# Kernel optimization log

Hardware: AMD Instinct MI355X
Metric: run time of the kernel (lower is better)

The kernel has to match this reference:

```python
import jax, jax.numpy as jnp
import numpy as np

B, S, D = 32, 512, 1024
H, HD = 16, 64          # num_heads, head_dim
K = 64                  # downsampling_k
NEG = -9e15             # -9000000000000000.0 in source


def setup_inputs() -> dict:
    key0 = jax.random.key(0)
    ks = jax.random.split(key0, 8)
    glorot = lambda k, shape, fan: jax.random.uniform(k, shape, jnp.float32,
                                                      -np.sqrt(6.0 / fan), np.sqrt(6.0 / fan))
    fan = D + H * HD  # glorot_uniform over (hidden, heads*head_dim)
    return {
        "query": jax.random.normal(ks[0], (B, S, D), jnp.float32),
        "key": jax.random.normal(ks[1], (B, S, D), jnp.float32),
        "value": jax.random.normal(ks[2], (B, S, D), jnp.float32),
        "query_kernel": glorot(ks[3], (D, H, HD), fan),
        "key_kernel": glorot(ks[4], (D, H, HD), fan),
        "value_kernel": glorot(ks[5], (D, H, HD), fan),
        "key_downsample_mat": (1.0 / K) * jax.random.normal(ks[6], (K, S), jnp.float32),
        "value_downsample_mat": (1.0 / K) * jax.random.normal(ks[7], (K, S), jnp.float32),
    }


def reference(query, key, value, query_kernel, key_kernel, value_kernel,
              key_downsample_mat, value_downsample_mat):
    # Linformer-style downsampling of K/V along the sequence axis: [B,S,D] -> [B,K,D]
    key_ds = jnp.einsum('ks,bsd->bkd', key_downsample_mat, key)
    val_ds = jnp.einsum('ks,bsd->bkd', value_downsample_mat, value)

    # Per-head projections
    q = jnp.einsum('bsd,dnh->bsnh', query, query_kernel)   # [B,S,H,HD]
    k = jnp.einsum('bkd,dnh->bknh', key_ds, key_kernel)    # [B,K,H,HD]
    v = jnp.einsum('bkd,dnh->bknh', val_ds, value_kernel)  # [B,K,H,HD]

    # Masked softmax attention over the downsampled key set
    scores = jnp.einsum('bqnh,bknh->bnqk', q, k)           # [B,H,S,K]
    # Source builds tril over [S, K_down] then slices first K cols (no-op here)
    mask = jnp.tril(jnp.ones((S, K), dtype=bool))          # [S,K], broadcasts over B,H
    scores = jnp.where(mask, scores, NEG)
    attn = jax.nn.softmax(scores, axis=-1)                 # dropout deterministic (train=False)

    a_v = jnp.einsum('bnqk,bknh->bqnh', attn, v)           # [B,S,H,HD]
    return a_v.reshape(B, S, H * HD)
```

## Files before the change

kernel.cpp:

```cpp
#include <hip/hip_runtime.h>
#include <stdint.h>

#define B_   32
#define S_   512
#define D_   1024
#define H_   16
#define HD_  64
#define KD_  64
#define NH_  1024

typedef __attribute__((ext_vector_type(8))) short short8;
typedef __attribute__((ext_vector_type(4))) float floatx4;

#define GAS __attribute__((address_space(1)))
#define LAS __attribute__((address_space(3)))

__device__ __forceinline__ ushort f2bf(float f) {
  uint32_t u = __float_as_uint(f);
  u = u + 0x7FFFu + ((u >> 16) & 1u);
  return (ushort)(u >> 16);
}

__device__ __forceinline__ float bf2f(ushort h) {
  return __uint_as_float(((uint32_t)h) << 16);
}

__device__ __forceinline__ void gload_lds16(const void* g, void* l) {
  __builtin_amdgcn_global_load_lds((const GAS uint32_t*)g, (LAS uint32_t*)l, 16, 0, 0);
}

#define BARRIER() asm volatile("s_barrier" ::: "memory")
#define WAITLGKM() asm volatile("s_waitcnt lgkmcnt(0)" ::: "memory")

__global__ __launch_bounds__(256) void cvt_split(const float* __restrict__ kdm,
                                                 const float* __restrict__ vdm,
                                                 ushort* __restrict__ hi,
                                                 ushort* __restrict__ lo) {
  int i = blockIdx.x * 256 + threadIdx.x;
  const float* src = (i < 8192) ? kdm : vdm;
  int j = i & 8191;
  float4 v = ((const float4*)src)[j];
  ushort4 h, l;
  h.x = f2bf(v.x); l.x = f2bf(v.x - bf2f(h.x));
  h.y = f2bf(v.y); l.y = f2bf(v.y - bf2f(h.y));
  h.z = f2bf(v.z); l.z = f2bf(v.z - bf2f(h.z));
  h.w = f2bf(v.w); l.w = f2bf(v.w - bf2f(h.w));
  ((ushort4*)hi)[i] = h;
  ((ushort4*)lo)[i] = l;
}

__global__ __launch_bounds__(256, 6) void pre_kv(
    const float* __restrict__ key, const float* __restrict__ value,
    const float* __restrict__ kkm, const float* __restrict__ vkm,
    const ushort* __restrict__ dsm_hi, const ushort* __restrict__ dsm_lo,
    ushort* __restrict__ kkT, ushort* __restrict__ vkT,
    ushort* __restrict__ outk, ushort* __restrict__ outv) {
  __shared__ __align__(16) char smem[26624];
  const int blk = blockIdx.x;
  const int tid = threadIdx.x;

  if (blk < 512) {
    const int bz = (blk & 7) + ((blk >> 6) << 3);
    const int t  = (blk >> 3) & 7;
    const int z = bz >> 5, b = bz & 31;
    const int c0 = t * 128;
    const float* in = z ? value : key;
    ushort* out     = z ? outv : outk;
    const ushort* Ah = dsm_hi + (size_t)z * (KD_ * S_);
    const ushort* Al = dsm_lo + (size_t)z * (KD_ * S_);

    ushort* lAh = (ushort*)smem;
    ushort* lAl = (ushort*)(smem + 4096);
    uint*   lBh = (uint*)(smem + 8192);
    uint*   lBl = (uint*)(smem + 17408);

    const int lane = tid & 63, w = tid >> 6;
    const int lr = lane & 15, lg = lane >> 4;
    const int wn = w * 32;
    const int lam = tid & 31;
    const int d0 = lam * 4;
    const int sp = tid >> 5;

    floatx4 acc[4][2];
#pragma unroll
    for (int m = 0; m < 4; ++m)
#pragma unroll
      for (int n = 0; n < 2; ++n) acc[m][n] = (floatx4){0.f, 0.f, 0.f, 0.f};

    for (int k0 = 0; k0 < S_; k0 += 32) {
      {
        size_t src = (size_t)(tid >> 2) * S_ + k0 + (size_t)(tid & 3) * 8;
        gload_lds16(Ah + src, lAh + w * 512);
        gload_lds16(Al + src, lAl + w * 512);
      }
      float4 ra[2], rb[2];
#pragma unroll
      for (int si = 0; si < 2; ++si) {
        int s = sp * 2 + si * 16;
        const float* p = in + ((size_t)(b * S_ + k0 + s)) * D_ + c0 + d0;
        ra[si] = *(const float4*)p;
        rb[si] = *(const float4*)(p + D_);
      }
      const int swz = lam & 12;
#pragma unroll
      for (int si = 0; si < 2; ++si) {
        int col = (sp + si * 8) ^ swz;
        const float* pa = (const float*)&ra[si];
        const float* pb = (const float*)&rb[si];
#pragma unroll
        for (int i = 0; i < 4; ++i) {
          ushort h0 = f2bf(pa[i]);
          ushort l0 = f2bf(pa[i] - bf2f(h0));
          ushort h1 = f2bf(pb[i]);
          ushort l1 = f2bf(pb[i] - bf2f(h1));
          lBh[(d0 + i) * 18 + col] = (uint)h0 | ((uint)h1 << 16);
          lBl[(d0 + i) * 18 + col] = (uint)l0 | ((uint)l1 << 16);
        }
      }
      __syncthreads();
      short8 bh[2], bl[2];
#pragma unroll
      for (int n = 0; n < 2; ++n) {
        int d = wn + n * 16 + lr;
        int off = d * 18 + ((lg * 4) ^ ((d >> 2) & 12));
        bh[n] = *(const short8*)&lBh[off];
        bl[n] = *(const short8*)&lBl[off];
      }
#pragma unroll
      for (int m = 0; m < 4; ++m) {
        int aoff = (m * 16 + lr) * 32 + lg * 8;
        short8 ah = *(const short8*)&lAh[aoff];
        short8 al = *(const short8*)&lAl[aoff];
#pragma unroll
        for (int n = 0; n < 2; ++n) {
          acc[m][n] = __builtin_amdgcn_mfma_f32_16x16x32_bf16(ah, bh[n], acc[m][n], 0, 0, 0);
          acc[m][n] = __builtin_amdgcn_mfma_f32_16x16x32_bf16(ah, bl[n], acc[m][n], 0, 0, 0);
          acc[m][n] = __builtin_amdgcn_mfma_f32_16x16x32_bf16(al, bh[n], acc[m][n], 0, 0, 0);
        }
      }
      __syncthreads();
    }
    size_t obase = (size_t)b * KD_ * D_;
#pragma unroll
    for (int m = 0; m < 4; ++m)
#pragma unroll
      for (int n = 0; n < 2; ++n)
#pragma unroll
        for (int r = 0; r < 4; ++r)
          out[obase + (size_t)(m * 16 + lg * 4 + r) * D_ + c0 + wn + n * 16 + lr] =
              f2bf(acc[m][n][r]);

  } else {
    const int blk2 = blk - 512;
    const int tz = blk2 >> 10;
    const int rem = blk2 & 1023;
    const int tyb = rem >> 5;
    const int txb = rem & 31;
    const float* in = tz == 0 ? kkm : vkm;
    ushort* outp    = tz == 0 ? kkT : vkT;
    float (*tile)[33] = (float(*)[33])smem;
    const int tx = tid & 31, ty = tid >> 5;
    int x = txb * 32 + tx;
    int y0 = tyb * 32;
#pragma unroll
    for (int j = 0; j < 4; ++j)
      tile[ty + j * 8][tx] = in[(size_t)(y0 + ty + j * 8) * 1024 + x];
    __syncthreads();
    int x2 = tyb * 32 + tx;
    int y2 = txb * 32;
#pragma unroll
    for (int j = 0; j < 4; ++j)
      outp[(size_t)(y2 + ty + j * 8) * 1024 + x2] = f2bf(tile[tx][ty + j * 8]);
  }
}

__global__ __launch_bounds__(256) void gemm_kv_q(
    const ushort* __restrict__ A,
    const ushort* __restrict__ Bt,
    const ushort* __restrict__ Bt2,
    ushort* __restrict__ C,
    const float* __restrict__ qk, ushort* __restrict__ qkT,
    const float* __restrict__ query, ushort* __restrict__ q_bf) {
  __shared__ __align__(16) char smem[16384];
  const int blk = blockIdx.x;
  const int tid = threadIdx.x;

  if (blk < 256) {
    ushort* lA = (ushort*)smem;
    ushort* lB = (ushort*)(smem + 8192);
    int xcd = blk & 7, slot = blk >> 3;
    int mt = xcd * 4 + (slot >> 3);
    int nt = slot & 7;
    int m0 = mt * 128, n0 = nt * 128;
    const ushort* Bsel = (mt >= 16) ? Bt2 : Bt;

    int lane = tid & 63, w = tid >> 6;
    int lr = lane & 15, lg = lane >> 4;
    int wm = (w >> 1) * 64, wn = (w & 1) * 64;
    floatx4 acc[4][4];
#pragma unroll
    for (int m = 0; m < 4; ++m)
#pragma unroll
      for (int n = 0; n < 4; ++n) acc[m][n] = (floatx4){0.f, 0.f, 0.f, 0.f};

    for (int k0 = 0; k0 < 1024; k0 += 32) {
#pragma unroll
      for (int i = 0; i < 2; ++i) {
        int c = i * 256 + w * 64 + lane;
        gload_lds16(A + ((size_t)(m0 + (c >> 2)) * 1024 + k0 + (c & 3) * 8),
                    &lA[(i * 256 + w * 64) * 8]);
        gload_lds16(Bsel + ((size_t)(n0 + (c >> 2)) * 1024 + k0 + (c & 3) * 8),
                    &lB[(i * 256 + w * 64) * 8]);
      }
      __syncthreads();
      short8 af[4], bfr[4];
#pragma unroll
      for (int m = 0; m < 4; ++m)
        af[m] = *(const short8*)&lA[(wm + m * 16 + lr) * 32 + lg * 8];
#pragma unroll
      for (int n = 0; n < 4; ++n)
        bfr[n] = *(const short8*)&lB[(wn + n * 16 + lr) * 32 + lg * 8];
#pragma unroll
      for (int m = 0; m < 4; ++m)
#pragma unroll
        for (int n = 0; n < 4; ++n)
          acc[m][n] = __builtin_amdgcn_mfma_f32_16x16x32_bf16(af[m], bfr[n], acc[m][n], 0, 0, 0);
      __syncthreads();
    }
#pragma unroll
    for (int m = 0; m < 4; ++m)
#pragma unroll
      for (int n = 0; n < 4; ++n)
#pragma unroll
        for (int r = 0; r < 4; ++r)
          C[(size_t)(m0 + wm + m * 16 + lg * 4 + r) * 1024 + n0 + wn + n * 16 + lr] =
              f2bf(acc[m][n][r]);

  } else if (blk < 256 + 1024) {
    const int blk2 = blk - 256;
    const int tyb = blk2 >> 5;
    const int txb = blk2 & 31;
    float (*tile)[33] = (float(*)[33])smem;
    const int tx = tid & 31, ty = tid >> 5;
    int x = txb * 32 + tx;
    int y0 = tyb * 32;
#pragma unroll
    for (int j = 0; j < 4; ++j)
      tile[ty + j * 8][tx] = qk[(size_t)(y0 + ty + j * 8) * 1024 + x];
    __syncthreads();
    int x2 = tyb * 32 + tx;
    int y2 = txb * 32;
#pragma unroll
    for (int j = 0; j < 4; ++j)
      qkT[(size_t)(y2 + ty + j * 8) * 1024 + x2] = f2bf(tile[tx][ty + j * 8]);

  } else {
    const size_t base = (size_t)(blk - 1280) * 2048 + tid;
#pragma unroll
    for (int j = 0; j < 8; ++j) {
      size_t i = base + (size_t)j * 256;
      float4 v = ((const float4*)query)[i];
      ushort4 o;
      o.x = f2bf(v.x); o.y = f2bf(v.y); o.z = f2bf(v.z); o.w = f2bf(v.w);
      ((ushort4*)q_bf)[i] = o;
    }
  }
}

__global__ __launch_bounds__(512, 2) void gemm256_attn(
    const ushort* __restrict__ A, const ushort* __restrict__ Bt,
    const ushort* __restrict__ kp, const ushort* __restrict__ vp,
    float* __restrict__ out) {
  extern __shared__ ushort lds[];
  ushort* ldsA = lds;
  ushort* ldsB = lds + 2 * 256 * 64;
  const int tid = threadIdx.x;
  const int w = tid >> 6, lane = tid & 63;
  const int lr = lane & 15, lg = lane >> 4;
  const int wm = w >> 2, wn = w & 3;
  const int bid = blockIdx.x;
  const int mt = (bid & 7) * 8 + ((bid >> 3) >> 2);
  const int nt = (bid >> 3) & 3;
  const int m0 = mt * 256, n0 = nt * 256;
  const int NT = 16;

  const int srow = tid >> 3;
  const int sslot = tid & 7;

  auto stageA = [&](int sl, int ch, int k0) {
    int rloc = ch * 64 + srow;
    int gs = sslot ^ (rloc & 7);
    gload_lds16(A + (size_t)(m0 + rloc) * 1024 + k0 + gs * 8,
                ldsA + sl * (256 * 64) + ch * (64 * 64) + w * 512);
  };
  auto stageB = [&](int sl, int ch, int k0) {
    int rloc = ch * 64 + srow;
    int gs = sslot ^ (rloc & 7);
    gload_lds16(Bt + (size_t)(n0 + rloc) * 1024 + k0 + gs * 8,
                ldsB + sl * (256 * 64) + ch * (64 * 64) + w * 512);
  };

  short8 af[4][2], bf[2][2];
  auto loadA = [&](int sl, int mh) {
#pragma unroll
    for (int i = 0; i < 4; ++i) {
      int row = wm * 128 + (mh * 4 + i) * 16 + lr;
#pragma unroll
      for (int kk = 0; kk < 2; ++kk) {
        int col = (((kk * 4 + lg) ^ (row & 7)) * 8);
        af[i][kk] = *(const short8*)&ldsA[sl * (256 * 64) + row * 64 + col];
      }
    }
  };
  auto loadB = [&](int sl, int nh) {
#pragma unroll
    for (int j = 0; j < 2; ++j) {
      int row = wn * 64 + (nh * 2 + j) * 16 + lr;
#pragma unroll
      for (int kk = 0; kk < 2; ++kk) {
        int col = (((kk * 4 + lg) ^ (row & 7)) * 8);
        bf[j][kk] = *(const short8*)&ldsB[sl * (256 * 64) + row * 64 + col];
      }
    }
  };

  floatx4 acc[8][4];
#pragma unroll
  for (int i = 0; i < 8; ++i)
#pragma unroll
    for (int j = 0; j < 4; ++j) acc[i][j] = (floatx4){0.f, 0.f, 0.f, 0.f};

  auto mma16 = [&](int mh, int nh) {
    __builtin_amdgcn_s_setprio(1);
#pragma unroll
    for (int i = 0; i < 4; ++i)
#pragma unroll
      for (int j = 0; j < 2; ++j)
#pragma unroll
        for (int kk = 0; kk < 2; ++kk)
          acc[mh * 4 + i][nh * 2 + j] = __builtin_amdgcn_mfma_f32_16x16x32_bf16(
              af[i][kk], bf[j][kk], acc[mh * 4 + i][nh * 2 + j], 0, 0, 0);
    __builtin_amdgcn_s_setprio(0);
  };

#pragma unroll
  for (int ch = 0; ch < 4; ++ch) { stageA(0, ch, 0); stageB(0, ch, 0); }

#pragma unroll 2
  for (int t = 0; t < NT; ++t) {
    const int s = t & 1, ns = s ^ 1;
    const int kn = (t + 1) << 6;
    const bool more = (t + 1 < NT);
    if (more) { stageA(ns, 0, kn); stageA(ns, 1, kn); }
    if (more) { asm volatile("s_waitcnt vmcnt(2)" ::: "memory"); }
    else      { asm volatile("s_waitcnt vmcnt(0)" ::: "memory"); }
    BARRIER();
    loadA(s, 0); loadB(s, 0);
    WAITLGKM();
    mma16(0, 0);
    BARRIER();
    loadB(s, 1);
    if (more) { stageB(ns, 0, kn); stageB(ns, 1, kn); }
    BARRIER();
    WAITLGKM();
    mma16(0, 1);
    BARRIER();
    loadA(s, 1);
    if (more) { stageA(ns, 2, kn); stageA(ns, 3, kn); }
    BARRIER();
    WAITLGKM();
    mma16(1, 1);
    BARRIER();
    loadB(s, 0);
    if (more) { stageB(ns, 2, kn); stageB(ns, 3, kn); }
    BARRIER();
    WAITLGKM();
    mma16(1, 0);
    BARRIER();
  }

  ushort* QP = lds + w * 4608;
  ushort* sV = lds + 8 * 4608;
  const int b = mt >> 1;
  const int hq = nt * 4 + wn;

  {
    int hh = tid >> 7, t2 = tid & 127;
    int k = t2 >> 1, h0 = (t2 & 1) * 32;
    const ushort* src = vp + ((size_t)b * KD_ + k) * 1024 + (nt * 4 + hh) * HD_ + h0;
#pragma unroll
    for (int i = 0; i < 32; ++i) sV[hh * 4608 + (h0 + i) * 72 + k] = src[i];
  }
  __syncthreads();

#pragma unroll
  for (int half = 0; half < 2; ++half) {
    const int srow0 = (mt & 1) * 256 + wm * 128 + half * 64;
#pragma unroll
    for (int mi = 0; mi < 4; ++mi)
#pragma unroll
      for (int nj = 0; nj < 4; ++nj)
#pragma unroll
        for (int r = 0; r < 4; ++r)
          QP[(mi * 16 + lg * 4 + r) * 72 + nj * 16 + lr] =
              f2bf(acc[half * 4 + mi][nj][r]);
    WAITLGKM();
    __builtin_amdgcn_sched_barrier(0);
    floatx4 qacc[4][4];
#pragma unroll
    for (int m = 0; m < 4; ++m)
#pragma unroll
      for (int n = 0; n < 4; ++n) qacc[m][n] = (floatx4){0.f, 0.f, 0.f, 0.f};
#pragma unroll
    for (int kk = 0; kk < 2; ++kk) {
      short8 qa[4], kb[4];
#pragma unroll
      for (int m = 0; m < 4; ++m)
        qa[m] = *(const short8*)&QP[(m * 16 + lr) * 72 + kk * 32 + lg * 8];
#pragma unroll
      for (int n = 0; n < 4; ++n)
        kb[n] = *(const short8*)(kp + ((size_t)b * KD_ + n * 16 + lr) * 1024 +
                                 hq * HD_ + kk * 32 + lg * 8);
#pragma unroll
      for (int m = 0; m < 4; ++m)
#pragma unroll
        for (int n = 0; n < 4; ++n)
          qacc[m][n] = __builtin_amdgcn_mfma_f32_16x16x32_bf16(qa[m], kb[n], qacc[m][n], 0, 0, 0);
    }
#pragma unroll
    for (int m = 0; m < 4; ++m) {
#pragma unroll
      for (int r = 0; r < 4; ++r) {
        int srow2 = srow0 + m * 16 + lg * 4 + r;
        float vals[4];
        float mx = -1e30f;
#pragma unroll
        for (int n = 0; n < 4; ++n) {
          int col = n * 16 + lr;
          float val = qacc[m][n][r];
          val = (col <= srow2) ? val : -1e30f;
          vals[n] = val;
          mx = fmaxf(mx, val);
        }
        mx = fmaxf(mx, __shfl_xor(mx, 1));
        mx = fmaxf(mx, __shfl_xor(mx, 2));
        mx = fmaxf(mx, __shfl_xor(mx, 4));
        mx = fmaxf(mx, __shfl_xor(mx, 8));
        float sum = 0.f;
#pragma unroll
        for (int n = 0; n < 4; ++n) {
          float e = __expf(vals[n] - mx);
          vals[n] = e;
          sum += e;
        }
        sum += __shfl_xor(sum, 1);
        sum += __shfl_xor(sum, 2);
        sum += __shfl_xor(sum, 4);
        sum += __shfl_xor(sum, 8);
        float inv = 1.0f / sum;
#pragma unroll
        for (int n = 0; n < 4; ++n)
          QP[(m * 16 + lg * 4 + r) * 72 + n * 16 + lr] = f2bf(vals[n] * inv);
      }
    }
    WAITLGKM();
    __builtin_amdgcn_sched_barrier(0);
    floatx4 oacc[4][4];
#pragma unroll
    for (int m = 0; m < 4; ++m)
#pragma unroll
      for (int n = 0; n < 4; ++n) oacc[m][n] = (floatx4){0.f, 0.f, 0.f, 0.f};
#pragma unroll
    for (int kk = 0; kk < 2; ++kk) {
      short8 pa[4], vb[4];
#pragma unroll
      for (int m = 0; m < 4; ++m)
        pa[m] = *(const short8*)&QP[(m * 16 + lr) * 72 + kk * 32 + lg * 8];
#pragma unroll
      for (int n = 0; n < 4; ++n)
        vb[n] = *(const short8*)&sV[wn * 4608 + (n * 16 + lr) * 72 + kk * 32 + lg * 8];
#pragma unroll
      for (int m = 0; m < 4; ++m)
#pragma unroll
        for (int n = 0; n < 4; ++n)
          oacc[m][n] = __builtin_amdgcn_mfma_f32_16x16x32_bf16(pa[m], vb[n], oacc[m][n], 0, 0, 0);
    }
#pragma unroll
    for (int m = 0; m < 4; ++m)
#pragma unroll
      for (int n = 0; n < 4; ++n)
#pragma unroll
        for (int r = 0; r < 4; ++r)
          out[((size_t)b * S_ + srow0 + m * 16 + lg * 4 + r) * 1024 +
              hq * HD_ + n * 16 + lr] = oacc[m][n][r];
  }
}

extern "C" void kernel_launch(void* const* d_in, const int* in_sizes, int n_in,
                              void* d_out, int out_size, void* d_ws, size_t ws_size,
                              hipStream_t stream) {
  const float* query = (const float*)d_in[0];
  const float* key   = (const float*)d_in[1];
  const float* value = (const float*)d_in[2];
  const float* qk    = (const float*)d_in[3];
  const float* kk    = (const float*)d_in[4];
  const float* vk    = (const float*)d_in[5];
  const float* kdm   = (const float*)d_in[6];
  const float* vdm   = (const float*)d_in[7];
  float* out = (float*)d_out;

  char* ws = (char*)d_ws;
  if (ws_size < (90ull << 20)) return;
  ushort* q_bf   = (ushort*)(ws);
  ushort* qkT    = (ushort*)(ws + (33ull << 20));
  ushort* kkT    = (ushort*)(ws + (35ull << 20));
  ushort* vkT    = (ushort*)(ws + (37ull << 20));
  ushort* kds    = (ushort*)(ws + (39ull << 20));
  ushort* vds    = (ushort*)(ws + (43ull << 20));
  ushort* k_proj = (ushort*)(ws + (79ull << 20));
  ushort* v_proj = (ushort*)(ws + (83ull << 20));
  ushort* dsm_hi = (ushort*)(ws + (87ull << 20));
  ushort* dsm_lo = (ushort*)(ws + (87ull << 20) + (128ull << 10));

  hipFuncSetAttribute((const void*)gemm256_attn,
                      hipFuncAttributeMaxDynamicSharedMemorySize, 131072);

  cvt_split<<<64, 256, 0, stream>>>(kdm, vdm, dsm_hi, dsm_lo);
  pre_kv<<<512 + 2048, 256, 0, stream>>>(
      key, value, kk, vk, dsm_hi, dsm_lo, kkT, vkT, kds, vds);
  gemm_kv_q<<<256 + 1024 + 2048, 256, 0, stream>>>(
      kds, kkT, vkT, k_proj, qk, qkT, query, q_bf);
  gemm256_attn<<<256, 512, 131072, stream>>>(q_bf, qkT, k_proj, v_proj, out);
}
```

Before: 129.6 us.

## Write projected V transposed in producer GEMM and read it directly in attention

The K/V projection GEMM now writes the V projection in a per-batch [head_dim, k] transposed layout using 4-wide stores. The attention kernel drops its scalar global-to-LDS transpose staging of V and the barrier after it, and loads V fragments straight from global memory as 16-byte vectors. This removes the strided scalar LDS transpose in the attention prologue. In exchange, every wave re-reads V fragments from global memory or cache on each half and each k-step instead of reading them from LDS.

Result: no change. 128.2 us (median of 3 runs) (-1.1%).

```diff
diff --git a/kernel.cpp b/kernel.cpp
--- a/kernel.cpp
+++ b/kernel.cpp
@@ -179,6 +179,7 @@
     const ushort* __restrict__ Bt,
     const ushort* __restrict__ Bt2,
     ushort* __restrict__ C,
+    ushort* __restrict__ vpT,
     const float* __restrict__ qk, ushort* __restrict__ qkT,
     const float* __restrict__ query, ushort* __restrict__ q_bf) {
   __shared__ __align__(16) char smem[16384];
@@ -227,14 +228,29 @@
           acc[m][n] = __builtin_amdgcn_mfma_f32_16x16x32_bf16(af[m], bfr[n], acc[m][n], 0, 0, 0);
       __syncthreads();
     }
-#pragma unroll
-    for (int m = 0; m < 4; ++m)
-#pragma unroll
-      for (int n = 0; n < 4; ++n)
-#pragma unroll
-        for (int r = 0; r < 4; ++r)
-          C[(size_t)(m0 + wm + m * 16 + lg * 4 + r) * 1024 + n0 + wn + n * 16 + lr] =
-              f2bf(acc[m][n][r]);
+    if (mt < 16) {
+#pragma unroll
+      for (int m = 0; m < 4; ++m)
+#pragma unroll
+        for (int n = 0; n < 4; ++n)
+#pragma unroll
+          for (int r = 0; r < 4; ++r)
+            C[(size_t)(m0 + wm + m * 16 + lg * 4 + r) * 1024 + n0 + wn + n * 16 + lr] =
+                f2bf(acc[m][n][r]);
+    } else {
+#pragma unroll
+      for (int m = 0; m < 4; ++m)
+#pragma unroll
+        for (int n = 0; n < 4; ++n) {
+          int rowV = m0 - 2048 + wm + m * 16 + lg * 4;
+          int b = rowV >> 6, k = rowV & 63;
+          int hd = n0 + wn + n * 16 + lr;
+          ushort4 o;
+          o.x = f2bf(acc[m][n][0]); o.y = f2bf(acc[m][n][1]);
+          o.z = f2bf(acc[m][n][2]); o.w = f2bf(acc[m][n][3]);
+          *(ushort4*)&vpT[(size_t)b * 65536 + (size_t)hd * 64 + k] = o;
+        }
+    }
 
   } else if (blk < 256 + 1024) {
     const int blk2 = blk - 256;
@@ -269,7 +285,7 @@
 
 __global__ __launch_bounds__(512, 2) void gemm256_attn(
     const ushort* __restrict__ A, const ushort* __restrict__ Bt,
-    const ushort* __restrict__ kp, const ushort* __restrict__ vp,
+    const ushort* __restrict__ kp, const ushort* __restrict__ vpT,
     float* __restrict__ out) {
   extern __shared__ ushort lds[];
   ushort* ldsA = lds;
@@ -380,18 +396,8 @@
   }
 
   ushort* QP = lds + w * 4608;
-  ushort* sV = lds + 8 * 4608;
   const int b = mt >> 1;
   const int hq = nt * 4 + wn;
-
-  {
-    int hh = tid >> 7, t2 = tid & 127;
-    int k = t2 >> 1, h0 = (t2 & 1) * 32;
-    const ushort* src = vp + ((size_t)b * KD_ + k) * 1024 + (nt * 4 + hh) * HD_ + h0;
-#pragma unroll
-    for (int i = 0; i < 32; ++i) sV[hh * 4608 + (h0 + i) * 72 + k] = src[i];
-  }
-  __syncthreads();
 
 #pragma unroll
   for (int half = 0; half < 2; ++half) {
@@ -478,7 +484,9 @@
         pa[m] = *(const short8*)&QP[(m * 16 + lr) * 72 + kk * 32 + lg * 8];
 #pragma unroll
       for (int n = 0; n < 4; ++n)
-        vb[n] = *(const short8*)&sV[wn * 4608 + (n * 16 + lr) * 72 + kk * 32 + lg * 8];
+        vb[n] = *(const short8*)(vpT + (size_t)b * 65536 +
+                                 (size_t)(hq * HD_ + n * 16 + lr) * 64 +
+                                 kk * 32 + lg * 8);
 #pragma unroll
       for (int m = 0; m < 4; ++m)
 #pragma unroll
@@ -518,7 +526,7 @@
   ushort* kds    = (ushort*)(ws + (39ull << 20));
   ushort* vds    = (ushort*)(ws + (43ull << 20));
   ushort* k_proj = (ushort*)(ws + (79ull << 20));
-  ushort* v_proj = (ushort*)(ws + (83ull << 20));
+  ushort* v_projT= (ushort*)(ws + (83ull << 20));
   ushort* dsm_hi = (ushort*)(ws + (87ull << 20));
   ushort* dsm_lo = (ushort*)(ws + (87ull << 20) + (128ull << 10));
 
@@ -529,6 +537,6 @@
   pre_kv<<<512 + 2048, 256, 0, stream>>>(
       key, value, kk, vk, dsm_hi, dsm_lo, kkT, vkT, kds, vds);
   gemm_kv_q<<<256 + 1024 + 2048, 256, 0, stream>>>(
-      kds, kkT, vkT, k_proj, qk, qkT, query, q_bf);
-  gemm256_attn<<<256, 512, 131072, stream>>>(q_bf, qkT, k_proj, v_proj, out);
-}
+      kds, kkT, vkT, k_proj, v_projT, qk, qkT, query, q_bf);
+  gemm256_attn<<<256, 512, 131072, stream>>>(q_bf, qkT, k_proj, v_projT, out);
+}
```
